# Kernel tuning notes

Hardware: AMD Instinct MI355X
Metric: run time of the kernel (lower is better)

The kernel has to match this reference:

```python
import jax, jax.numpy as jnp
import numpy as np

B, T, N, E = 4, 30, 2000, 32000
F_IN, F_HID, F_GRU, N_CLS = 8, 64, 128, 2


def setup_inputs() -> dict:
    key = jax.random.key(0)
    ks = jax.random.split(key, 12)
    return {
        "x": jax.random.normal(ks[0], (B, T, N, F_IN), jnp.float32),
        "edge_index": jax.random.randint(ks[1], (B, T, 2, E), 0, N, jnp.int32),
        "W1": jax.random.normal(ks[2], (F_IN, F_HID), jnp.float32) * 0.1,
        "b1": jax.random.normal(ks[3], (F_HID,), jnp.float32) * 0.1,
        "W2": jax.random.normal(ks[4], (F_HID, F_HID), jnp.float32) * 0.1,
        "b2": jax.random.normal(ks[5], (F_HID,), jnp.float32) * 0.1,
        "W_ih": jax.random.normal(ks[6], (3 * F_GRU, F_HID), jnp.float32) * 0.1,
        "W_hh": jax.random.normal(ks[7], (3 * F_GRU, F_GRU), jnp.float32) * 0.1,
        "b_ih": jax.random.normal(ks[8], (3 * F_GRU,), jnp.float32) * 0.1,
        "b_hh": jax.random.normal(ks[9], (3 * F_GRU,), jnp.float32) * 0.1,
        "fc_w": jax.random.normal(ks[10], (N_CLS, F_GRU), jnp.float32) * 0.1,
        "fc_b": jax.random.normal(ks[11], (N_CLS,), jnp.float32) * 0.1,
    }


def _gcn_conv(x, src, dst, W, b):
    # PyG GCNConv (edge_weight=None): add self-loops, sym-normalize, x@W, scatter-add, +bias
    n = x.shape[0]
    loops = jnp.arange(n, dtype=src.dtype)
    s = jnp.concatenate([src, loops])
    d = jnp.concatenate([dst, loops])
    deg = jax.ops.segment_sum(jnp.ones(s.shape[0], x.dtype), d, num_segments=n)
    dis = jnp.where(deg > 0, jax.lax.rsqrt(deg), 0.0)
    norm = dis[s] * dis[d]                      # [E+N]
    h = x @ W                                   # [N, Fout]
    msg = h[s] * norm[:, None]                  # gather + scale
    return jax.ops.segment_sum(msg, d, num_segments=n) + b


def _frame_embed(x, ei, W1, b1, W2, b2):
    # one graph frame -> mean-pooled 64-d embedding
    src, dst = ei[0], ei[1]
    h = jax.nn.relu(_gcn_conv(x, src, dst, W1, b1))
    h = jax.nn.relu(_gcn_conv(h, src, dst, W2, b2))
    return h.mean(axis=0)


def _gru(H, W_ih, W_hh, b_ih, b_hh):
    # H: [T, B, F_HID]; torch GRU gate order: r, z, n
    def step(h, x_t):
        gi = x_t @ W_ih.T + b_ih                # [B, 3H]
        gh = h @ W_hh.T + b_hh
        i_r, i_z, i_n = jnp.split(gi, 3, axis=-1)
        h_r, h_z, h_n = jnp.split(gh, 3, axis=-1)
        r = jax.nn.sigmoid(i_r + h_r)
        z = jax.nn.sigmoid(i_z + h_z)
        n = jnp.tanh(i_n + r * h_n)
        h_new = (1.0 - z) * n + z * h
        return h_new, None
    h0 = jnp.zeros((H.shape[1], F_GRU), H.dtype)
    h_final, _ = jax.lax.scan(step, h0, H)
    return h_final                              # [B, F_GRU]


def reference(x, edge_index, W1, b1, W2, b2, W_ih, W_hh, b_ih, b_hh, fc_w, fc_b):
    G = B * T
    xf = x.reshape(G, N, F_IN)
    eif = edge_index.reshape(G, 2, E)
    emb = jax.vmap(_frame_embed, in_axes=(0, 0, None, None, None, None))(
        xf, eif, W1, b1, W2, b2)                # [G, 64]
    H = emb.reshape(B, T, F_HID).transpose(1, 0, 2)  # [T, B, 64]
    h_final = _gru(H, W_ih, W_hh, b_ih, b_hh)   # [B, 128]
    return h_final @ fc_w.T + fc_b              # [B, 2]
```

## Files before the change

### kernel.cpp

```cpp
#include <hip/hip_runtime.h>
#include <math.h>

#define G    120
#define Nn   2000
#define Ee   32000
#define Tt   30
#define Bb   4
#define Fg   128
#define QCAP 9216
#define TSLOT 48

static __device__ __forceinline__ unsigned short f2bf(float f) {
    unsigned u = __float_as_uint(f);
    u += 0x7fffu + ((u >> 16) & 1u);
    return (unsigned short)(u >> 16);
}

#if defined(__has_builtin)
#if __has_builtin(__builtin_amdgcn_cvt_f32_fp8) && __has_builtin(__builtin_amdgcn_cvt_pk_fp8_f32)
#define HW_FP8 1
#endif
#if __has_builtin(__builtin_amdgcn_cvt_pk_f32_fp8)
#define HW_FP8_PK 1
typedef float floatx2 __attribute__((ext_vector_type(2)));
#endif
#endif

static __device__ __forceinline__ unsigned fp8_enc_sw(float x) {
    unsigned s = (__float_as_uint(x) >> 24) & 0x80u;
    float ax = fminf(fabsf(x), 448.f);
    unsigned em;
    if (ax < 0.015625f) {
        em = (unsigned)__float2int_rn(ax * 512.f);
    } else {
        int e = (int)(__float_as_uint(ax) >> 23) - 127;
        float r = ax * __uint_as_float((unsigned)((130 - e) << 23));
        int q = __float2int_rn(r);
        em = (unsigned)(((e + 7) << 3) + (q - 8));
        em = min(em, 126u);
    }
    return s | em;
}
static __device__ __forceinline__ float fp8_dec_sw(unsigned b) {
    unsigned em = b & 0x7fu;
    float mag;
    if (em < 8u) mag = (float)em * 0.001953125f;
    else mag = __uint_as_float((((em >> 3) + 120u) << 23) | ((em & 7u) << 20));
    return (b & 0x80u) ? -mag : mag;
}
static __device__ __forceinline__ unsigned fp8_pack4(float a, float b, float c, float d) {
#ifdef HW_FP8
    int w = __builtin_amdgcn_cvt_pk_fp8_f32(a, b, 0, false);
    w = __builtin_amdgcn_cvt_pk_fp8_f32(c, d, w, true);
    return (unsigned)w;
#else
    return fp8_enc_sw(a) | (fp8_enc_sw(b) << 8) | (fp8_enc_sw(c) << 16) | (fp8_enc_sw(d) << 24);
#endif
}
static __device__ __forceinline__ void fp8x4_dec(unsigned dw, float* o) {
#ifdef HW_FP8_PK
    floatx2 lo = __builtin_amdgcn_cvt_pk_f32_fp8((int)dw, false);
    floatx2 hi = __builtin_amdgcn_cvt_pk_f32_fp8((int)dw, true);
    o[0] = lo[0]; o[1] = lo[1]; o[2] = hi[0]; o[3] = hi[1];
#else
    o[0] = fp8_dec_sw(dw & 0xffu);
    o[1] = fp8_dec_sw((dw >> 8) & 0xffu);
    o[2] = fp8_dec_sw((dw >> 16) & 0xffu);
    o[3] = fp8_dec_sw((dw >> 24) & 0xffu);
#endif
}

__global__ void __launch_bounds__(1024, 1)
k_build(const int* __restrict__ ei, float* __restrict__ dis,
        int* __restrict__ startA, int* __restrict__ cntA,
        int* __restrict__ csr, unsigned* __restrict__ ellT,
        int* __restrict__ cntS, int* __restrict__ ordS,
        float* __restrict__ emb) {
    __shared__ int   hist[Nn];
    __shared__ float disl[Nn];
    __shared__ int   ws[512];
    __shared__ int   csr_l[QCAP];
    __shared__ int   cntQ[500];
    __shared__ int   exQ[500];
    __shared__ int   nodeAt[500];
    __shared__ int   dh[64];
    __shared__ int   db[64];
    __shared__ int   ovfS;
    int i = blockIdx.x;
    int xcd = i & 7;
    int j = i >> 3;
    int f15 = j >> 2;
    int q = j & 3;
    int g = xcd * 15 + f15;
    int gq = g * 4 + q;
    int lo = q * 500;
    int tid = threadIdx.x;
    for (int idx = tid; idx < Nn; idx += 1024) hist[idx] = 0;
    if (tid < 64) dh[tid] = 0;
    if (tid == 0) ovfS = 0;
    if (q == 0 && tid < 64) emb[g * 64 + tid] = 0.f;
    __syncthreads();
    const int* srcp = ei + (size_t)g * 2 * Ee;
    const int* dstp = srcp + Ee;
    for (int it = tid; it < Ee / 4; it += 1024) {
        int4 d = reinterpret_cast<const int4*>(dstp)[it];
        atomicAdd(&hist[d.x], 1);
        atomicAdd(&hist[d.y], 1);
        atomicAdd(&hist[d.z], 1);
        atomicAdd(&hist[d.w], 1);
    }
    __syncthreads();
    for (int idx = tid; idx < Nn; idx += 1024) disl[idx] = rsqrtf((float)hist[idx] + 1.0f);
    int cnt = 0;
    if (tid < 512) ws[tid] = (tid < 500) ? hist[lo + tid] : 0;
    if (tid < 500) cnt = hist[lo + tid];
    __syncthreads();
    for (int off = 1; off < 512; off <<= 1) {
        int v = 0;
        if (tid < 512 && tid >= off) v = ws[tid - off];
        __syncthreads();
        if (tid < 512) ws[tid] += v;
        __syncthreads();
    }
    int ex = 0;
    if (tid < 500) ex = ws[tid] - cnt;
    if (tid < 500) {
        hist[lo + tid] = ex;
        cntQ[tid] = cnt;
        exQ[tid] = ex;
        if (cnt > TSLOT - 1) atomicMax(&ovfS, 1);
        atomicAdd(&dh[min(cnt, 63)], 1);
    }
    __syncthreads();
    if (tid == 0) {
        int s = 0;
        for (int b = 0; b < 64; ++b) { db[b] = s; s += dh[b]; }
    }
    __syncthreads();
    if (tid < 64) dh[tid] = db[tid];
    __syncthreads();
    if (tid < 500) {
        int p = atomicAdd(&dh[min(cnt, 63)], 1);
        nodeAt[p] = tid;
    }
    for (int it = tid; it < Ee / 4; it += 1024) {
        int4 d = reinterpret_cast<const int4*>(dstp)[it];
        int4 s = reinterpret_cast<const int4*>(srcp)[it];
        if (d.x >= lo && d.x < lo + 500) { int p = atomicAdd(&hist[d.x], 1); if (p < QCAP) csr_l[p] = s.x; }
        if (d.y >= lo && d.y < lo + 500) { int p = atomicAdd(&hist[d.y], 1); if (p < QCAP) csr_l[p] = s.y; }
        if (d.z >= lo && d.z < lo + 500) { int p = atomicAdd(&hist[d.z], 1); if (p < QCAP) csr_l[p] = s.z; }
        if (d.w >= lo && d.w < lo + 500) { int p = atomicAdd(&hist[d.w], 1); if (p < QCAP) csr_l[p] = s.w; }
    }
    __syncthreads();
    if (tid < 500) {
        int n_own = lo + tid;
        size_t gn_own = (size_t)g * Nn + n_own;
        cntA[gn_own] = cnt;
        startA[gn_own] = gq * QCAP + ex;
        dis[gn_own] = disl[n_own];
        int sl = nodeAt[tid];
        int n2 = lo + sl;
        int cnt2 = cntQ[sl];
        int ex2 = exQ[sl];
        int c = q * 500 + tid;
        size_t gc = (size_t)g * Nn + c;
        cntS[gc] = cnt2;
        ordS[gc] = n2;
        float dn2 = disl[n2];
        unsigned* et = ellT + (size_t)g * TSLOT * Nn + c;
        et[0] = (unsigned)n2 | ((unsigned)f2bf(dn2 * dn2) << 16);
        int m2 = min(cnt2, TSLOT - 1);
        for (int e = 0; e < m2; ++e) {
            int s = csr_l[ex2 + e];
            et[(size_t)(e + 1) * Nn] = (unsigned)s | ((unsigned)f2bf(disl[s] * dn2) << 16);
        }
    }
    __syncthreads();
    if (ovfS) {
        int total = ws[511];
        int* cg = csr + (size_t)gq * QCAP;
        for (int it = tid; it < total; it += 1024) cg[it] = csr_l[it];
    }
}

__global__ void __launch_bounds__(256)
k_fused(const float* __restrict__ x, const unsigned* __restrict__ ellT,
        const int* __restrict__ cntS, const int* __restrict__ ordS,
        const int* __restrict__ startA, const int* __restrict__ csr,
        const float* __restrict__ dis,
        const float* __restrict__ W1, const float* __restrict__ b1,
        const float* __restrict__ W2, unsigned char* __restrict__ t2f) {
    int i = blockIdx.x;
    int xcd = i & 7;
    int j = i >> 3;
    int g = xcd * 15 + (j >> 3);
    int blk = j & 7;
    int p = blk * 256 + threadIdx.x;
    bool valid = (p < Nn);
    size_t gp = (size_t)g * Nn + (valid ? p : 0);
    int n = valid ? ordS[gp] : 0;
    int cnt = valid ? cntS[gp] : 0;
    int myc = valid ? (min(cnt, TSLOT - 1) + 1) : 0;
    float aX[8];
#pragma unroll
    for (int k = 0; k < 8; ++k) aX[k] = 0.f;
    {
        const unsigned* et = ellT + (size_t)g * TSLOT * Nn + (valid ? p : 0);
        const float4* x4 = reinterpret_cast<const float4*>(x + (size_t)g * Nn * 8);
        unsigned ub[8], nb[8];
#pragma unroll
        for (int k = 0; k < 8; ++k)
            ub[k] = (k < myc) ? et[(size_t)k * Nn] : 0u;
        for (int e0 = 0; e0 < TSLOT; e0 += 8) {
            bool more = (e0 + 8 < TSLOT) && __any(e0 + 8 < myc);
            if (more) {
#pragma unroll
                for (int k = 0; k < 8; ++k)
                    nb[k] = (e0 + 8 + k < myc) ? et[(size_t)(e0 + 8 + k) * Nn] : 0u;
            }
#pragma unroll
            for (int k = 0; k < 8; ++k) {
                if (e0 + k < myc) {
                    float w = __uint_as_float(ub[k] & 0xffff0000u);
                    int s = ub[k] & 0xffffu;
                    float4 r0 = x4[s * 2], r1 = x4[s * 2 + 1];
                    aX[0] += r0.x * w; aX[1] += r0.y * w; aX[2] += r0.z * w; aX[3] += r0.w * w;
                    aX[4] += r1.x * w; aX[5] += r1.y * w; aX[6] += r1.z * w; aX[7] += r1.w * w;
                }
            }
            if (!more) break;
#pragma unroll
            for (int k = 0; k < 8; ++k) ub[k] = nb[k];
        }
        if (cnt > TSLOT - 1) {
            size_t gn = (size_t)g * Nn + n;
            float dn = dis[gn];
            int start = startA[gn];
            const float* dsg = dis + (size_t)g * Nn;
            for (int e = TSLOT - 1; e < cnt; ++e) {
                int s = csr[start + e];
                float w = dsg[s] * dn;
                float4 r0 = x4[s * 2], r1 = x4[s * 2 + 1];
                aX[0] += r0.x * w; aX[1] += r0.y * w; aX[2] += r0.z * w; aX[3] += r0.w * w;
                aX[4] += r1.x * w; aX[5] += r1.y * w; aX[6] += r1.z * w; aX[7] += r1.w * w;
            }
        }
    }
    float h1r[64];
    {
        const float4* b14 = reinterpret_cast<const float4*>(b1);
#pragma unroll
        for (int f4 = 0; f4 < 16; ++f4) {
            float4 b = b14[f4];
            h1r[4 * f4 + 0] = b.x; h1r[4 * f4 + 1] = b.y;
            h1r[4 * f4 + 2] = b.z; h1r[4 * f4 + 3] = b.w;
        }
        const float4* W14 = reinterpret_cast<const float4*>(W1);
#pragma unroll
        for (int k = 0; k < 8; ++k) {
            float hk = aX[k];
#pragma unroll
            for (int f4 = 0; f4 < 16; ++f4) {
                float4 w = W14[k * 16 + f4];
                h1r[4 * f4 + 0] += hk * w.x; h1r[4 * f4 + 1] += hk * w.y;
                h1r[4 * f4 + 2] += hk * w.z; h1r[4 * f4 + 3] += hk * w.w;
            }
        }
#pragma unroll
        for (int f = 0; f < 64; ++f) h1r[f] = fmaxf(h1r[f], 0.f);
    }
    uint4 oh[2][2];
    {
        const float4* W24 = reinterpret_cast<const float4*>(W2);
#pragma unroll
        for (int hf = 0; hf < 2; ++hf) {
            float acch[32];
#pragma unroll
            for (int f = 0; f < 32; ++f) acch[f] = 0.f;
#pragma unroll
            for (int k = 0; k < 64; ++k) {
                float hk = h1r[k];
#pragma unroll
                for (int f4 = 0; f4 < 8; ++f4) {
                    float4 w = W24[k * 16 + hf * 8 + f4];
                    acch[4 * f4 + 0] += hk * w.x; acch[4 * f4 + 1] += hk * w.y;
                    acch[4 * f4 + 2] += hk * w.z; acch[4 * f4 + 3] += hk * w.w;
                }
            }
            oh[hf][0].x = fp8_pack4(acch[0],  acch[1],  acch[2],  acch[3]);
            oh[hf][0].y = fp8_pack4(acch[4],  acch[5],  acch[6],  acch[7]);
            oh[hf][0].z = fp8_pack4(acch[8],  acch[9],  acch[10], acch[11]);
            oh[hf][0].w = fp8_pack4(acch[12], acch[13], acch[14], acch[15]);
            oh[hf][1].x = fp8_pack4(acch[16], acch[17], acch[18], acch[19]);
            oh[hf][1].y = fp8_pack4(acch[20], acch[21], acch[22], acch[23]);
            oh[hf][1].z = fp8_pack4(acch[24], acch[25], acch[26], acch[27]);
            oh[hf][1].w = fp8_pack4(acch[28], acch[29], acch[30], acch[31]);
        }
    }
    if (valid) {
        uint4* op = reinterpret_cast<uint4*>(t2f + ((size_t)g * Nn + n) * 64);
        op[0] = oh[0][0]; op[1] = oh[0][1]; op[2] = oh[1][0]; op[3] = oh[1][1];
    }
}

__global__ void __launch_bounds__(1024, 1)
k_aggF(const unsigned char* __restrict__ t2f, const unsigned* __restrict__ ellT,
       const int* __restrict__ cntS, const int* __restrict__ ordS,
       const int* __restrict__ startA, const int* __restrict__ csr,
       const float* __restrict__ dis, const float* __restrict__ bias,
       float* __restrict__ emb) {
    __shared__ uint4 stage[Nn * 5];
    int i = blockIdx.x;
    int xcd = i & 7;
    int j = i >> 3;
    int g = xcd * 15 + (j >> 1);
    int half = j & 1;
    int tid = threadIdx.x;
    int w = tid >> 6, lane = tid & 63;
    {
        const uint4* src = reinterpret_cast<const uint4*>(t2f + (size_t)g * Nn * 64);
        for (int it = tid; it < Nn * 4; it += 1024)
            stage[(it >> 2) * 5 + (it & 3)] = src[it];
    }
    __syncthreads();
#define ROWFMA(dw, base) { float o_[4]; fp8x4_dec(dw, o_); \
    acc[base + 0] += o_[0] * wt; acc[base + 1] += o_[1] * wt; \
    acc[base + 2] += o_[2] * wt; acc[base + 3] += o_[3] * wt; }
    int po = w * 64 + lane;
    int p = half * 1000 + po;
    bool valid = (po < 1000);
    size_t gp = (size_t)g * Nn + (valid ? p : 0);
    int cnt = valid ? cntS[gp] : 0;
    int myc = valid ? (min(cnt, TSLOT - 1) + 1) : 0;
    float acc[64];
#pragma unroll
    for (int k = 0; k < 64; ++k) acc[k] = 0.f;
    const unsigned* et = ellT + (size_t)g * TSLOT * Nn + (valid ? p : 0);
    for (int e = 0; e < TSLOT; ++e) {
        if (!__any(e < myc)) break;
        if (e < myc) {
            unsigned u = et[(size_t)e * Nn];
            float wt = __uint_as_float(u & 0xffff0000u);
            int s = u & 0xffffu;
            uint4 r0 = stage[s * 5], r1 = stage[s * 5 + 1];
            uint4 r2 = stage[s * 5 + 2], r3 = stage[s * 5 + 3];
            ROWFMA(r0.x, 0)  ROWFMA(r0.y, 4)  ROWFMA(r0.z, 8)  ROWFMA(r0.w, 12)
            ROWFMA(r1.x, 16) ROWFMA(r1.y, 20) ROWFMA(r1.z, 24) ROWFMA(r1.w, 28)
            ROWFMA(r2.x, 32) ROWFMA(r2.y, 36) ROWFMA(r2.z, 40) ROWFMA(r2.w, 44)
            ROWFMA(r3.x, 48) ROWFMA(r3.y, 52) ROWFMA(r3.z, 56) ROWFMA(r3.w, 60)
        }
    }
    if (cnt > TSLOT - 1) {
        int n = ordS[gp];
        size_t gn = (size_t)g * Nn + n;
        float dn = dis[gn];
        int start = startA[gn];
        const float* dsg = dis + (size_t)g * Nn;
        for (int e = TSLOT - 1; e < cnt; ++e) {
            int s = csr[start + e];
            float wt = dsg[s] * dn;
            uint4 r0 = stage[s * 5], r1 = stage[s * 5 + 1];
            uint4 r2 = stage[s * 5 + 2], r3 = stage[s * 5 + 3];
            ROWFMA(r0.x, 0)  ROWFMA(r0.y, 4)  ROWFMA(r0.z, 8)  ROWFMA(r0.w, 12)
            ROWFMA(r1.x, 16) ROWFMA(r1.y, 20) ROWFMA(r1.z, 24) ROWFMA(r1.w, 28)
            ROWFMA(r2.x, 32) ROWFMA(r2.y, 36) ROWFMA(r2.z, 40) ROWFMA(r2.w, 44)
            ROWFMA(r3.x, 48) ROWFMA(r3.y, 52) ROWFMA(r3.z, 56) ROWFMA(r3.w, 60)
        }
    }
#undef ROWFMA
    float pool = 0.f;
#pragma unroll
    for (int k = 0; k < 64; ++k) {
        float v = valid ? fmaxf(acc[k] + bias[k], 0.f) : 0.f;
        v += __shfl_xor(v, 1);  v += __shfl_xor(v, 2);  v += __shfl_xor(v, 4);
        v += __shfl_xor(v, 8);  v += __shfl_xor(v, 16); v += __shfl_xor(v, 32);
        if (lane == k) pool = v;
    }
    atomicAdd(&emb[g * 64 + lane], pool * (1.0f / Nn));
}

__global__ void k_gi(const float* __restrict__ emb, const float* __restrict__ W_ih,
                     const float* __restrict__ b_ih, float* __restrict__ gi) {
    __shared__ float xs[64];
    int g = blockIdx.x;
    int j = threadIdx.x;
    if (j < 64) xs[j] = emb[g * 64 + j];
    __syncthreads();
    float a0 = 0.f, a1 = 0.f, a2 = 0.f, a3 = 0.f;
    const float* wr = W_ih + j * 64;
#pragma unroll
    for (int k = 0; k < 16; ++k) {
        a0 += wr[4 * k + 0] * xs[4 * k + 0];
        a1 += wr[4 * k + 1] * xs[4 * k + 1];
        a2 += wr[4 * k + 2] * xs[4 * k + 2];
        a3 += wr[4 * k + 3] * xs[4 * k + 3];
    }
    gi[(size_t)g * 384 + j] = b_ih[j] + ((a0 + a1) + (a2 + a3));
}

__global__ void __launch_bounds__(768, 1)
k_gru_seq(const float* __restrict__ gi, const float* __restrict__ W_hh,
          const float* __restrict__ b_hh, const float* __restrict__ fc_w,
          const float* __restrict__ fc_b, float* __restrict__ out) {
    __shared__ float h[Fg];
    __shared__ float part[768];
    int b = blockIdx.x;
    int tid = threadIdx.x;
    int row = tid >> 1;
    int half = tid & 1;
    float w[64];
    const float* wr = W_hh + (size_t)row * Fg + half * 64;
#pragma unroll
    for (int i = 0; i < 64; ++i) w[i] = wr[i];
    if (tid < Fg) h[tid] = 0.f;
    __syncthreads();
    for (int t = 0; t < Tt; ++t) {
        const float* hh = &h[half * 64];
        float a0 = 0.f, a1 = 0.f, a2 = 0.f, a3 = 0.f;
#pragma unroll
        for (int i = 0; i < 16; ++i) {
            a0 += w[4 * i + 0] * hh[4 * i + 0];
            a1 += w[4 * i + 1] * hh[4 * i + 1];
            a2 += w[4 * i + 2] * hh[4 * i + 2];
            a3 += w[4 * i + 3] * hh[4 * i + 3];
        }
        part[tid] = (a0 + a1) + (a2 + a3);
        __syncthreads();
        if (tid < Fg) {
            int j = tid;
            const float* gib = gi + ((size_t)b * Tt + t) * 384;
            float hr = b_hh[j]       + part[2 * j]           + part[2 * j + 1];
            float hz = b_hh[128 + j] + part[2 * (128 + j)]   + part[2 * (128 + j) + 1];
            float hn = b_hh[256 + j] + part[2 * (256 + j)]   + part[2 * (256 + j) + 1];
            float r  = 1.f / (1.f + expf(-(gib[j] + hr)));
            float z  = 1.f / (1.f + expf(-(gib[128 + j] + hz)));
            float nn = tanhf(gib[256 + j] + r * hn);
            h[j] = (1.f - z) * nn + z * h[j];
        }
        __syncthreads();
    }
    if (tid < 2) {
        float acc = fc_b[tid];
        for (int k = 0; k < Fg; ++k) acc += fc_w[tid * Fg + k] * h[k];
        out[b * 2 + tid] = acc;
    }
}

extern "C" void kernel_launch(void* const* d_in, const int* in_sizes, int n_in,
                              void* d_out, int out_size, void* d_ws, size_t ws_size,
                              hipStream_t stream) {
    const float* x     = (const float*)d_in[0];
    const int*   ei    = (const int*)  d_in[1];
    const float* W1    = (const float*)d_in[2];
    const float* b1    = (const float*)d_in[3];
    const float* W2    = (const float*)d_in[4];
    const float* b2    = (const float*)d_in[5];
    const float* W_ih  = (const float*)d_in[6];
    const float* W_hh  = (const float*)d_in[7];
    const float* b_ih  = (const float*)d_in[8];
    const float* b_hh  = (const float*)d_in[9];
    const float* fc_w  = (const float*)d_in[10];
    const float* fc_b  = (const float*)d_in[11];
    float* out = (float*)d_out;

    char* ws = (char*)d_ws;
    size_t off = 0;
    auto alloc = [&](size_t bytes) -> void* {
        void* p = ws + off;
        off = (off + bytes + 255) & ~(size_t)255;
        return p;
    };
    float*    dis    = (float*)   alloc((size_t)G * Nn * 4);
    int*      startA = (int*)     alloc((size_t)G * Nn * 4);
    int*      cntA   = (int*)     alloc((size_t)G * Nn * 4);
    int*      cntS   = (int*)     alloc((size_t)G * Nn * 4);
    int*      ordS   = (int*)     alloc((size_t)G * Nn * 4);
    int*      csr    = (int*)     alloc((size_t)G * 4 * QCAP * 4);
    unsigned* ellT   = (unsigned*)alloc((size_t)G * TSLOT * Nn * 4);
    unsigned char* t2f = (unsigned char*)alloc((size_t)G * Nn * 64);
    float*    emb    = (float*)   alloc((size_t)G * 64 * 4);
    float*    gi     = (float*)   alloc((size_t)G * 384 * 4);
    (void)ws_size; (void)in_sizes; (void)n_in; (void)out_size;

    hipLaunchKernelGGL(k_build,   dim3(480), dim3(1024), 0, stream, ei, dis, startA, cntA, csr, ellT, cntS, ordS, emb);
    hipLaunchKernelGGL(k_fused,   dim3(960), dim3(256), 0, stream, x, ellT, cntS, ordS, startA, csr, dis, W1, b1, W2, t2f);
    hipLaunchKernelGGL(k_aggF,    dim3(240), dim3(1024), 0, stream, t2f, ellT, cntS, ordS, startA, csr, dis, b2, emb);
    hipLaunchKernelGGL(k_gi,      dim3(G), dim3(384), 0, stream, emb, W_ih, b_ih, gi);
    hipLaunchKernelGGL(k_gru_seq, dim3(Bb), dim3(768), 0, stream, gi, W_hh, b_hh, fc_w, fc_b, out);
}
```

Baseline: 261.3 us.

## Stage frame features in LDS for layer-1 gather and fuse input GRU gates

```diff
diff --git a/kernel.cpp b/kernel.cpp
--- a/kernel.cpp
+++ b/kernel.cpp
@@ -190,11 +190,21 @@
         const float* __restrict__ dis,
         const float* __restrict__ W1, const float* __restrict__ b1,
         const float* __restrict__ W2, unsigned char* __restrict__ t2f) {
+    __shared__ float xs[8][Nn];
     int i = blockIdx.x;
     int xcd = i & 7;
     int j = i >> 3;
     int g = xcd * 15 + (j >> 3);
     int blk = j & 7;
+    {
+        const float4* x4 = reinterpret_cast<const float4*>(x + (size_t)g * Nn * 8);
+        for (int it = threadIdx.x; it < Nn; it += 256) {
+            float4 r0 = x4[it * 2], r1 = x4[it * 2 + 1];
+            xs[0][it] = r0.x; xs[1][it] = r0.y; xs[2][it] = r0.z; xs[3][it] = r0.w;
+            xs[4][it] = r1.x; xs[5][it] = r1.y; xs[6][it] = r1.z; xs[7][it] = r1.w;
+        }
+    }
+    __syncthreads();
     int p = blk * 256 + threadIdx.x;
     bool valid = (p < Nn);
     size_t gp = (size_t)g * Nn + (valid ? p : 0);
@@ -206,31 +216,23 @@
     for (int k = 0; k < 8; ++k) aX[k] = 0.f;
     {
         const unsigned* et = ellT + (size_t)g * TSLOT * Nn + (valid ? p : 0);
-        const float4* x4 = reinterpret_cast<const float4*>(x + (size_t)g * Nn * 8);
-        unsigned ub[8], nb[8];
-#pragma unroll
-        for (int k = 0; k < 8; ++k)
-            ub[k] = (k < myc) ? et[(size_t)k * Nn] : 0u;
         for (int e0 = 0; e0 < TSLOT; e0 += 8) {
-            bool more = (e0 + 8 < TSLOT) && __any(e0 + 8 < myc);
-            if (more) {
-#pragma unroll
-                for (int k = 0; k < 8; ++k)
-                    nb[k] = (e0 + 8 + k < myc) ? et[(size_t)(e0 + 8 + k) * Nn] : 0u;
-            }
+            if (!__any(e0 < myc)) break;
+            unsigned ub[8];
+#pragma unroll
+            for (int k = 0; k < 8; ++k)
+                ub[k] = (e0 + k < myc) ? et[(size_t)(e0 + k) * Nn] : 0u;
 #pragma unroll
             for (int k = 0; k < 8; ++k) {
                 if (e0 + k < myc) {
                     float w = __uint_as_float(ub[k] & 0xffff0000u);
                     int s = ub[k] & 0xffffu;
-                    float4 r0 = x4[s * 2], r1 = x4[s * 2 + 1];
-                    aX[0] += r0.x * w; aX[1] += r0.y * w; aX[2] += r0.z * w; aX[3] += r0.w * w;
-                    aX[4] += r1.x * w; aX[5] += r1.y * w; aX[6] += r1.z * w; aX[7] += r1.w * w;
+                    aX[0] += xs[0][s] * w; aX[1] += xs[1][s] * w;
+                    aX[2] += xs[2][s] * w; aX[3] += xs[3][s] * w;
+                    aX[4] += xs[4][s] * w; aX[5] += xs[5][s] * w;
+                    aX[6] += xs[6][s] * w; aX[7] += xs[7][s] * w;
                 }
             }
-            if (!more) break;
-#pragma unroll
-            for (int k = 0; k < 8; ++k) ub[k] = nb[k];
         }
         if (cnt > TSLOT - 1) {
             size_t gn = (size_t)g * Nn + n;
@@ -240,9 +242,10 @@
             for (int e = TSLOT - 1; e < cnt; ++e) {
                 int s = csr[start + e];
                 float w = dsg[s] * dn;
-                float4 r0 = x4[s * 2], r1 = x4[s * 2 + 1];
-                aX[0] += r0.x * w; aX[1] += r0.y * w; aX[2] += r0.z * w; aX[3] += r0.w * w;
-                aX[4] += r1.x * w; aX[5] += r1.y * w; aX[6] += r1.z * w; aX[7] += r1.w * w;
+                aX[0] += xs[0][s] * w; aX[1] += xs[1][s] * w;
+                aX[2] += xs[2][s] * w; aX[3] += xs[3][s] * w;
+                aX[4] += xs[4][s] * w; aX[5] += xs[5][s] * w;
+                aX[6] += xs[6][s] * w; aX[7] += xs[7][s] * w;
             }
         }
     }
@@ -379,31 +382,15 @@
     atomicAdd(&emb[g * 64 + lane], pool * (1.0f / Nn));
 }
 
-__global__ void k_gi(const float* __restrict__ emb, const float* __restrict__ W_ih,
-                     const float* __restrict__ b_ih, float* __restrict__ gi) {
-    __shared__ float xs[64];
-    int g = blockIdx.x;
-    int j = threadIdx.x;
-    if (j < 64) xs[j] = emb[g * 64 + j];
-    __syncthreads();
-    float a0 = 0.f, a1 = 0.f, a2 = 0.f, a3 = 0.f;
-    const float* wr = W_ih + j * 64;
-#pragma unroll
-    for (int k = 0; k < 16; ++k) {
-        a0 += wr[4 * k + 0] * xs[4 * k + 0];
-        a1 += wr[4 * k + 1] * xs[4 * k + 1];
-        a2 += wr[4 * k + 2] * xs[4 * k + 2];
-        a3 += wr[4 * k + 3] * xs[4 * k + 3];
-    }
-    gi[(size_t)g * 384 + j] = b_ih[j] + ((a0 + a1) + (a2 + a3));
-}
-
 __global__ void __launch_bounds__(768, 1)
-k_gru_seq(const float* __restrict__ gi, const float* __restrict__ W_hh,
+k_gru_seq(const float* __restrict__ emb, const float* __restrict__ W_ih,
+          const float* __restrict__ b_ih, const float* __restrict__ W_hh,
           const float* __restrict__ b_hh, const float* __restrict__ fc_w,
           const float* __restrict__ fc_b, float* __restrict__ out) {
     __shared__ float h[Fg];
     __shared__ float part[768];
+    __shared__ float embs[Tt][64];
+    __shared__ float pgi[Tt][768];
     int b = blockIdx.x;
     int tid = threadIdx.x;
     int row = tid >> 1;
@@ -412,7 +399,26 @@
     const float* wr = W_hh + (size_t)row * Fg + half * 64;
 #pragma unroll
     for (int i = 0; i < 64; ++i) w[i] = wr[i];
+    float wih[32];
+    const float* wir = W_ih + (size_t)row * 64 + half * 32;
+#pragma unroll
+    for (int i = 0; i < 32; ++i) wih[i] = wir[i];
+    for (int it = tid; it < Tt * 64; it += 768)
+        embs[it >> 6][it & 63] = emb[((size_t)b * Tt) * 64 + it];
     if (tid < Fg) h[tid] = 0.f;
+    __syncthreads();
+    for (int t = 0; t < Tt; ++t) {
+        const float* e = &embs[t][half * 32];
+        float a0 = 0.f, a1 = 0.f, a2 = 0.f, a3 = 0.f;
+#pragma unroll
+        for (int i = 0; i < 8; ++i) {
+            a0 += wih[4 * i + 0] * e[4 * i + 0];
+            a1 += wih[4 * i + 1] * e[4 * i + 1];
+            a2 += wih[4 * i + 2] * e[4 * i + 2];
+            a3 += wih[4 * i + 3] * e[4 * i + 3];
+        }
+        pgi[t][tid] = (a0 + a1) + (a2 + a3);
+    }
     __syncthreads();
     for (int t = 0; t < Tt; ++t) {
         const float* hh = &h[half * 64];
@@ -428,13 +434,15 @@
         __syncthreads();
         if (tid < Fg) {
             int j = tid;
-            const float* gib = gi + ((size_t)b * Tt + t) * 384;
             float hr = b_hh[j]       + part[2 * j]           + part[2 * j + 1];
             float hz = b_hh[128 + j] + part[2 * (128 + j)]   + part[2 * (128 + j) + 1];
             float hn = b_hh[256 + j] + part[2 * (256 + j)]   + part[2 * (256 + j) + 1];
-            float r  = 1.f / (1.f + expf(-(gib[j] + hr)));
-            float z  = 1.f / (1.f + expf(-(gib[128 + j] + hz)));
-            float nn = tanhf(gib[256 + j] + r * hn);
+            float gr = b_ih[j]       + pgi[t][2 * j]         + pgi[t][2 * j + 1];
+            float gz = b_ih[128 + j] + pgi[t][2 * (128 + j)] + pgi[t][2 * (128 + j) + 1];
+            float gn = b_ih[256 + j] + pgi[t][2 * (256 + j)] + pgi[t][2 * (256 + j) + 1];
+            float r  = 1.f / (1.f + expf(-(gr + hr)));
+            float z  = 1.f / (1.f + expf(-(gz + hz)));
+            float nn = tanhf(gn + r * hn);
             h[j] = (1.f - z) * nn + z * h[j];
         }
         __syncthreads();
@@ -479,12 +487,10 @@
     unsigned* ellT   = (unsigned*)alloc((size_t)G * TSLOT * Nn * 4);
     unsigned char* t2f = (unsigned char*)alloc((size_t)G * Nn * 64);
     float*    emb    = (float*)   alloc((size_t)G * 64 * 4);
-    float*    gi     = (float*)   alloc((size_t)G * 384 * 4);
     (void)ws_size; (void)in_sizes; (void)n_in; (void)out_size;
 
     hipLaunchKernelGGL(k_build,   dim3(480), dim3(1024), 0, stream, ei, dis, startA, cntA, csr, ellT, cntS, ordS, emb);
     hipLaunchKernelGGL(k_fused,   dim3(960), dim3(256), 0, stream, x, ellT, cntS, ordS, startA, csr, dis, W1, b1, W2, t2f);
     hipLaunchKernelGGL(k_aggF,    dim3(240), dim3(1024), 0, stream, t2f, ellT, cntS, ordS, startA, csr, dis, b2, emb);
-    hipLaunchKernelGGL(k_gi,      dim3(G), dim3(384), 0, stream, emb, W_ih, b_ih, gi);
-    hipLaunchKernelGGL(k_gru_seq, dim3(Bb), dim3(768), 0, stream, gi, W_hh, b_hh, fc_w, fc_b, out);
-}
+    hipLaunchKernelGGL(k_gru_seq, dim3(Bb), dim3(768), 0, stream, emb, W_ih, b_ih, W_hh, b_hh, fc_w, fc_b, out);
+}
```

After: 283.2 us. 8.4% more time.
